# Optimization experiments

Measured on AMD Instinct MI355X. Metric: run time of the kernel, lower is better.

Reference implementation:

```python
import jax, jax.numpy as jnp
import numpy as np

IN_MODES = (8, 8, 8, 8)
OUT_MODES = (8, 8, 8, 8)
R = 16
RANKS = (1, R, R, R, 1)
BATCH = 8192
PROD_IN = int(np.prod(IN_MODES))   # 4096
PROD_OUT = int(np.prod(OUT_MODES))  # 4096


def setup_inputs() -> dict:
    key = jax.random.key(0)
    ks = jax.random.split(key, 6)
    # matches reset_normal() init scale
    CONST = ((0.05 ** 2 / np.prod(RANKS)) ** (1.0 / (len(RANKS) - 1))) ** 0.5
    P0 = jax.random.normal(ks[0], (OUT_MODES[0] * IN_MODES[0], R, 1), jnp.float32) * CONST
    P1 = jax.random.normal(ks[1], (OUT_MODES[1] * IN_MODES[1], R, R), jnp.float32) * CONST
    P2 = jax.random.normal(ks[2], (OUT_MODES[2] * IN_MODES[2], R, R), jnp.float32) * CONST
    P3 = jax.random.normal(ks[3], (OUT_MODES[3] * IN_MODES[3], R, 1), jnp.float32) * CONST
    bias = jnp.zeros((PROD_OUT,), jnp.float32)
    x = jax.random.normal(ks[5], (BATCH, PROD_IN), jnp.float32)
    return {"x": x, "P0": P0, "P1": P1, "P2": P2, "P3": P3, "bias": bias}


def _cayley(P):
    # Batched Cayley transform: Q = (I - A) @ inv(I + A), A skew from triu(P,1).
    # P: (n, r, r)
    T = jnp.triu(P, 1)
    A = T - jnp.swapaxes(T, -1, -2)
    I = jnp.eye(P.shape[-1], dtype=P.dtype)
    return jnp.einsum('nij,njk->nik', I - A, jnp.linalg.inv(I + A))


def _core(Q, o, m, r_in, r_out, first):
    # Q: (o*m, r, c) stacked in (j, k) order -> U: (r, o, m, c) as in getU
    r, c = Q.shape[1], Q.shape[2]
    U = Q.reshape(o, m, r, c).transpose(2, 0, 1, 3)  # (r, o, m, c)
    if first:
        U = jnp.swapaxes(U, 0, 3)  # (c=1, o, m, r)
    return U.reshape(o * r_out, m * r_in)  # G_i: (o_i * ranks[i+1], m_i * ranks[i])


def _build_cores(P0, P1, P2, P3):
    G0 = _core(P0, OUT_MODES[0], IN_MODES[0], RANKS[0], RANKS[1], True)
    G1 = _core(_cayley(P1), OUT_MODES[1], IN_MODES[1], RANKS[1], RANKS[2], False)
    G2 = _core(_cayley(P2), OUT_MODES[2], IN_MODES[2], RANKS[2], RANKS[3], False)
    G3 = _core(P3, OUT_MODES[3], IN_MODES[3], RANKS[3], RANKS[4], False)
    return [G0, G1, G2, G3]


def _tt_dot(x, G, bias):
    res = x.reshape(-1, PROD_IN).T  # (prod_in, B)
    for ii in range(4):
        res = res.reshape(RANKS[ii] * IN_MODES[ii], -1)
        res = G[ii] @ res                       # (o_i * r_{i+1}, rest)
        res = res.reshape(OUT_MODES[ii], -1).T  # rotate processed mode to back
    res = res.reshape(-1, PROD_OUT)
    return res + bias


def reference(x, P0, P1, P2, P3, bias):
    G = _build_cores(P0, P1, P2, P3)
    return _tt_dot(x, G, bias)
```

## Files before the change

kernel.cpp:

```cpp
#include <hip/hip_runtime.h>
#include <hip/hip_bf16.h>

typedef __attribute__((ext_vector_type(8))) short sh8;
typedef __attribute__((ext_vector_type(16))) float fx16;
typedef __attribute__((ext_vector_type(4))) unsigned int u32x4;

__device__ __forceinline__ unsigned short f2bits(float a) {
  union { __hip_bfloat16 h; unsigned short u; } c;
  c.h = __float2bfloat16(a);
  return c.u;
}
__device__ __forceinline__ unsigned int pkcvt(float a, float b) {
  unsigned int r;
  asm("v_cvt_pk_bf16_f32 %0, %1, %2" : "=v"(r) : "v"(a), "v"(b));
  return r;
}
__device__ __forceinline__ fx16 fzero16() {
  fx16 z;
  #pragma unroll
  for (int i = 0; i < 16; ++i) z[i] = 0.0f;
  return z;
}

__global__ void k_cayley(const float* __restrict__ P1, const float* __restrict__ P2,
                         float* __restrict__ Qout) {
  int t = blockIdx.x * blockDim.x + threadIdx.x;
  int mat = t >> 4;
  int row = t & 15;
  if (mat >= 128) return;
  const float* P = (mat < 64) ? (P1 + mat * 256) : (P2 + (mat - 64) * 256);
  float M[16], Rr[16];
  #pragma unroll
  for (int j = 0; j < 16; ++j) {
    float a = 0.0f;
    if (j > row) a = P[row * 16 + j];
    if (j < row) a = -P[j * 16 + row];
    float d = (j == row) ? 1.0f : 0.0f;
    M[j]  = d + a;
    Rr[j] = d - a;
  }
  int gbase = (threadIdx.x & 63) & ~15;
  #pragma unroll
  for (int k = 0; k < 16; ++k) {
    float pkk = __shfl(M[k], gbase + k);
    float inv = 1.0f / pkk;
    float pM[16], pR[16];
    #pragma unroll
    for (int j = 0; j < 16; ++j) {
      pM[j] = __shfl(M[j], gbase + k) * inv;
      pR[j] = __shfl(Rr[j], gbase + k) * inv;
    }
    if (row == k) {
      #pragma unroll
      for (int j = 0; j < 16; ++j) { M[j] = pM[j]; Rr[j] = pR[j]; }
    } else {
      float f = M[k];
      #pragma unroll
      for (int j = 0; j < 16; ++j) { M[j] -= f * pM[j]; Rr[j] -= f * pR[j]; }
    }
  }
  float* qo = Qout + mat * 256 + row * 16;
  #pragma unroll
  for (int j = 0; j < 16; ++j) qo[j] = Rr[j];
}

__global__ void k_build(const float* __restrict__ P0, const float* __restrict__ P3,
                        const float* __restrict__ Qbuf,
                        unsigned short* __restrict__ W1, unsigned short* __restrict__ W2) {
  int t = blockIdx.x * blockDim.x + threadIdx.x;
  if (t >= 131072) return;
  const float* Q1 = Qbuf;
  const float* Q2 = Qbuf + 16384;
  int e  = t & 65535;
  int r  = e & 7;
  int l  = (e >> 3) & 63;
  int kx = (e >> 9) & 3;
  int mt = (e >> 11) & 1;
  int t2 = (e >> 12) & 15;
  float acc = 0.0f;
  if (t < 65536) {
    int m = mt * 32 + (l & 31);
    int q = kx * 16 + ((l >> 5) << 3) + r;
    int j0 = m >> 3, j1 = m & 7, i0 = q >> 3, i1 = q & 7;
    #pragma unroll
    for (int t1 = 0; t1 < 16; ++t1) {
      float c0 = P0[(j0 * 8 + (t1 >> 1)) * 16 + ((t1 & 1) * 8 + i0)];
      int a1 = j1 * 16 + t2, u1 = t1 * 8 + i1;
      float c1 = Q1[((a1 & 7) * 8 + (u1 >> 4)) * 256 + (a1 >> 3) * 16 + (u1 & 15)];
      acc += c0 * c1;
    }
    W1[e] = f2bits(acc);
  } else {
    int n = mt * 32 + (l & 31);
    int s = kx * 16 + (r & 3) + 8 * (r >> 2) + 4 * (l >> 5);
    int j2 = n >> 3, j3 = n & 7, i2 = s >> 3, i3 = s & 7;
    #pragma unroll
    for (int t3 = 0; t3 < 16; ++t3) {
      int a2 = j2 * 16 + t3, u2 = t2 * 8 + i2;
      float c2 = Q2[((a2 & 7) * 8 + (u2 >> 4)) * 256 + (a2 >> 3) * 16 + (u2 & 15)];
      float c3 = P3[((t3 & 7) * 8 + i3) * 16 + (j3 * 2 + (t3 >> 3))];
      acc += c2 * c3;
    }
    W2[e] = f2bits(acc);
  }
}

__global__ __launch_bounds__(256, 2) void k_main(
    const float* __restrict__ x,
    const unsigned short* __restrict__ W1,
    const unsigned short* __restrict__ W2,
    const float* __restrict__ bias,
    float* __restrict__ out) {
  __shared__ __align__(16) char smem[4 * 8192 + 2 * 16384];
  char* XsT = smem;
  char* WL  = smem + 32768;

  const int tid  = threadIdx.x;
  const int lane = tid & 63;
  const int w    = tid >> 6;
  const int h    = lane >> 5;
  const int l31  = lane & 31;
  const int ep   = (w >> 1) * 2;
  const int mh   = w & 1;
  const size_t bbase = (size_t)blockIdx.x * 4;

  const char* w1c = (const char*)W1;
  const char* w2c = (const char*)W2;

  {
    char* dst = WL;
    #pragma unroll
    for (int c = 0; c < 4; ++c) {
      const char* src = (c < 2) ? (w1c + c * 4096) : (w2c + (c - 2) * 4096);
      src += w * 1024 + lane * 16;
      __builtin_amdgcn_global_load_lds((const unsigned int*)src,
                                       (unsigned int*)(dst + c * 4096 + w * 1024),
                                       16, 0, 0);
    }
  }

  {
    const int s = lane;
    const float* xb = x + (bbase + w) * 4096;
    const unsigned sw = ((unsigned)(s & 7)) << 4;
    char* base = XsT + w * 8192 + s * 128;
    #pragma unroll
    for (int c = 0; c < 4; ++c) {
      unsigned int d[8];
      #pragma unroll
      for (int jj = 0; jj < 8; ++jj) {
        float a  = xb[(c * 16 + 2 * jj + 0) * 64 + s];
        float bq = xb[(c * 16 + 2 * jj + 1) * 64 + s];
        d[jj] = pkcvt(a, bq);
      }
      u32x4 v0 = {d[0], d[1], d[2], d[3]};
      u32x4 v1 = {d[4], d[5], d[6], d[7]};
      *(u32x4*)(base + (((unsigned)(c * 32)) ^ sw))      = v0;
      *(u32x4*)(base + (((unsigned)(c * 32 + 16)) ^ sw)) = v1;
    }
  }
  asm volatile("s_waitcnt vmcnt(0)" ::: "memory");
  __syncthreads();

  sh8 af[2][2][4];
  #pragma unroll
  for (int e = 0; e < 2; ++e) {
    const char* myX = XsT + (ep + e) * 8192;
    #pragma unroll
    for (int st = 0; st < 2; ++st)
      #pragma unroll
      for (int kq = 0; kq < 4; ++kq) {
        int srow = st * 32 + l31;
        unsigned boff = (unsigned)srow * 128 +
                        (((unsigned)(kq * 32 + h * 16)) ^ (((unsigned)(srow & 7)) << 4));
        af[e][st][kq] = *(const sh8*)(myX + boff);
      }
  }

  const fx16 zc = fzero16();
  fx16 accO[2][2];
  accO[0][0] = zc; accO[0][1] = zc;
  accO[1][0] = zc; accO[1][1] = zc;

  #pragma unroll 1
  for (int t2 = 0; t2 < 16; ++t2) {
    char* cur = WL + (t2 & 1) * 16384;

    if (t2 < 15) {
      char* dst = WL + ((t2 + 1) & 1) * 16384;
      const size_t toff = (size_t)(t2 + 1) * 8192;
      #pragma unroll
      for (int c = 0; c < 4; ++c) {
        const char* src = (c < 2) ? (w1c + toff + c * 4096)
                                  : (w2c + toff + (c - 2) * 4096);
        src += w * 1024 + lane * 16;
        __builtin_amdgcn_global_load_lds((const unsigned int*)src,
                                         (unsigned int*)(dst + c * 4096 + w * 1024),
                                         16, 0, 0);
      }
    }

    sh8 b1[4];
    #pragma unroll
    for (int kq = 0; kq < 4; ++kq)
      b1[kq] = *(const sh8*)(cur + (((mh * 4 + kq) * 64 + lane) << 4));

    fx16 accY[2], accZ[2];
    __builtin_amdgcn_s_setprio(1);
    accY[0] = __builtin_amdgcn_mfma_f32_32x32x16_bf16(af[0][0][0], b1[0], zc, 0, 0, 0);
    accY[1] = __builtin_amdgcn_mfma_f32_32x32x16_bf16(af[0][1][0], b1[0], zc, 0, 0, 0);
    accZ[0] = __builtin_amdgcn_mfma_f32_32x32x16_bf16(af[1][0][0], b1[0], zc, 0, 0, 0);
    accZ[1] = __builtin_amdgcn_mfma_f32_32x32x16_bf16(af[1][1][0], b1[0], zc, 0, 0, 0);
    #pragma unroll
    for (int kq = 1; kq < 4; ++kq) {
      accY[0] = __builtin_amdgcn_mfma_f32_32x32x16_bf16(af[0][0][kq], b1[kq], accY[0], 0, 0, 0);
      accY[1] = __builtin_amdgcn_mfma_f32_32x32x16_bf16(af[0][1][kq], b1[kq], accY[1], 0, 0, 0);
      accZ[0] = __builtin_amdgcn_mfma_f32_32x32x16_bf16(af[1][0][kq], b1[kq], accZ[0], 0, 0, 0);
      accZ[1] = __builtin_amdgcn_mfma_f32_32x32x16_bf16(af[1][1][kq], b1[kq], accZ[1], 0, 0, 0);
    }
    __builtin_amdgcn_s_setprio(0);

    sh8 b2[2][4];
    #pragma unroll
    for (int nt = 0; nt < 2; ++nt)
      #pragma unroll
      for (int ks = 0; ks < 4; ++ks)
        b2[nt][ks] = *(const sh8*)(cur + 8192 + (((nt * 4 + ks) * 64 + lane) << 4));

    sh8 ga0[4], ga1[4];
    #pragma unroll
    for (int st = 0; st < 2; ++st) {
      fx16 Y = accY[st];
      union { u32x4 u; sh8 s8; } c0, c1;
      c0.u = (u32x4){pkcvt(Y[0], Y[1]),  pkcvt(Y[2], Y[3]),
                     pkcvt(Y[4], Y[5]),  pkcvt(Y[6], Y[7])};
      c1.u = (u32x4){pkcvt(Y[8], Y[9]),  pkcvt(Y[10], Y[11]),
                     pkcvt(Y[12], Y[13]), pkcvt(Y[14], Y[15])};
      ga0[st * 2 + 0] = c0.s8;
      ga0[st * 2 + 1] = c1.s8;
    }
    #pragma unroll
    for (int st = 0; st < 2; ++st) {
      fx16 Y = accZ[st];
      union { u32x4 u; sh8 s8; } c0, c1;
      c0.u = (u32x4){pkcvt(Y[0], Y[1]),  pkcvt(Y[2], Y[3]),
                     pkcvt(Y[4], Y[5]),  pkcvt(Y[6], Y[7])};
      c1.u = (u32x4){pkcvt(Y[8], Y[9]),  pkcvt(Y[10], Y[11]),
                     pkcvt(Y[12], Y[13]), pkcvt(Y[14], Y[15])};
      ga1[st * 2 + 0] = c0.s8;
      ga1[st * 2 + 1] = c1.s8;
    }

    __builtin_amdgcn_s_setprio(1);
    #pragma unroll
    for (int ks = 0; ks < 4; ++ks) {
      accO[0][0] = __builtin_amdgcn_mfma_f32_32x32x16_bf16(ga0[ks], b2[0][ks], accO[0][0], 0, 0, 0);
      accO[0][1] = __builtin_amdgcn_mfma_f32_32x32x16_bf16(ga0[ks], b2[1][ks], accO[0][1], 0, 0, 0);
      accO[1][0] = __builtin_amdgcn_mfma_f32_32x32x16_bf16(ga1[ks], b2[0][ks], accO[1][0], 0, 0, 0);
      accO[1][1] = __builtin_amdgcn_mfma_f32_32x32x16_bf16(ga1[ks], b2[1][ks], accO[1][1], 0, 0, 0);
    }
    __builtin_amdgcn_s_setprio(0);

    asm volatile("s_waitcnt vmcnt(0)" ::: "memory");
    __syncthreads();
  }

  #pragma unroll
  for (int e = 0; e < 2; ++e) {
    float* ob = out + (bbase + ep + e) * 4096;
    #pragma unroll
    for (int nt = 0; nt < 2; ++nt) {
      #pragma unroll
      for (int reg = 0; reg < 16; ++reg) {
        int m = mh * 32 + (reg & 3) + 8 * (reg >> 2) + 4 * h;
        int n = nt * 32 + l31;
        int o = m * 64 + n;
        ob[o] = accO[e][nt][reg] + bias[o];
      }
    }
  }
}

extern "C" void kernel_launch(void* const* d_in, const int* in_sizes, int n_in,
                              void* d_out, int out_size, void* d_ws, size_t ws_size,
                              hipStream_t stream) {
  (void)n_in; (void)out_size; (void)ws_size;
  const float* x    = (const float*)d_in[0];
  const float* P0   = (const float*)d_in[1];
  const float* P1   = (const float*)d_in[2];
  const float* P2   = (const float*)d_in[3];
  const float* P3   = (const float*)d_in[4];
  const float* bias = (const float*)d_in[5];
  float* out = (float*)d_out;

  float* Qbuf = (float*)d_ws;
  unsigned short* W1 = (unsigned short*)((char*)d_ws + 131072);
  unsigned short* W2 = (unsigned short*)((char*)d_ws + 262144);

  k_cayley<<<8, 256, 0, stream>>>(P1, P2, Qbuf);
  k_build<<<512, 256, 0, stream>>>(P0, P3, Qbuf, W1, W2);

  int batch = in_sizes[0] / 4096;
  k_main<<<batch / 4, 256, 0, stream>>>(x, W1, W2, bias, out);
}
```

Before: 137.7 us.

## Software-pipeline second-stage MFMAs across iterations and reload X fragments from LDS

The main loop is restructured so the second-stage GEMM (accO updates) for tile t-1 is interleaved with the first-stage GEMM for tile t, with a peeled prologue and epilogue. This gives independent MFMA chains to overlap instead of back-to-back dependent ones. The A fragments of X are no longer held in registers for the whole kernel; they are re-read from LDS each iteration per batch element, which lowers register pressure but adds LDS traffic. The b2 fragments are carried across iterations in registers.

```diff
diff --git a/kernel.cpp b/kernel.cpp
--- a/kernel.cpp
+++ b/kernel.cpp
@@ -162,37 +162,34 @@
   asm volatile("s_waitcnt vmcnt(0)" ::: "memory");
   __syncthreads();
 
-  sh8 af[2][2][4];
-  #pragma unroll
-  for (int e = 0; e < 2; ++e) {
-    const char* myX = XsT + (ep + e) * 8192;
-    #pragma unroll
-    for (int st = 0; st < 2; ++st)
-      #pragma unroll
-      for (int kq = 0; kq < 4; ++kq) {
-        int srow = st * 32 + l31;
-        unsigned boff = (unsigned)srow * 128 +
-                        (((unsigned)(kq * 32 + h * 16)) ^ (((unsigned)(srow & 7)) << 4));
-        af[e][st][kq] = *(const sh8*)(myX + boff);
-      }
-  }
+  unsigned aoff[2][4];
+  #pragma unroll
+  for (int st = 0; st < 2; ++st)
+    #pragma unroll
+    for (int kq = 0; kq < 4; ++kq) {
+      int srow = st * 32 + l31;
+      aoff[st][kq] = (unsigned)srow * 128 +
+                     (((unsigned)(kq * 32 + h * 16)) ^ (((unsigned)(srow & 7)) << 4));
+    }
+  const char* myX0 = XsT + (ep + 0) * 8192;
+  const char* myX1 = XsT + (ep + 1) * 8192;
 
   const fx16 zc = fzero16();
   fx16 accO[2][2];
   accO[0][0] = zc; accO[0][1] = zc;
   accO[1][0] = zc; accO[1][1] = zc;
 
-  #pragma unroll 1
-  for (int t2 = 0; t2 < 16; ++t2) {
-    char* cur = WL + (t2 & 1) * 16384;
-
-    if (t2 < 15) {
-      char* dst = WL + ((t2 + 1) & 1) * 16384;
-      const size_t toff = (size_t)(t2 + 1) * 8192;
+  sh8 ga0[4], ga1[4];
+  sh8 b2h[2][4];
+
+  {
+    char* cur = WL;
+    {
+      char* dst = WL + 16384;
       #pragma unroll
       for (int c = 0; c < 4; ++c) {
-        const char* src = (c < 2) ? (w1c + toff + c * 4096)
-                                  : (w2c + toff + (c - 2) * 4096);
+        const char* src = (c < 2) ? (w1c + 8192 + c * 4096)
+                                  : (w2c + 8192 + (c - 2) * 4096);
         src += w * 1024 + lane * 16;
         __builtin_amdgcn_global_load_lds((const unsigned int*)src,
                                          (unsigned int*)(dst + c * 4096 + w * 1024),
@@ -205,29 +202,46 @@
     for (int kq = 0; kq < 4; ++kq)
       b1[kq] = *(const sh8*)(cur + (((mh * 4 + kq) * 64 + lane) << 4));
 
+    sh8 afc[2][4];
+    #pragma unroll
+    for (int st = 0; st < 2; ++st)
+      #pragma unroll
+      for (int kq = 0; kq < 4; ++kq)
+        afc[st][kq] = *(const sh8*)(myX0 + aoff[st][kq]);
+
     fx16 accY[2], accZ[2];
     __builtin_amdgcn_s_setprio(1);
-    accY[0] = __builtin_amdgcn_mfma_f32_32x32x16_bf16(af[0][0][0], b1[0], zc, 0, 0, 0);
-    accY[1] = __builtin_amdgcn_mfma_f32_32x32x16_bf16(af[0][1][0], b1[0], zc, 0, 0, 0);
-    accZ[0] = __builtin_amdgcn_mfma_f32_32x32x16_bf16(af[1][0][0], b1[0], zc, 0, 0, 0);
-    accZ[1] = __builtin_amdgcn_mfma_f32_32x32x16_bf16(af[1][1][0], b1[0], zc, 0, 0, 0);
+    accY[0] = __builtin_amdgcn_mfma_f32_32x32x16_bf16(afc[0][0], b1[0], zc, 0, 0, 0);
+    accY[1] = __builtin_amdgcn_mfma_f32_32x32x16_bf16(afc[1][0], b1[0], zc, 0, 0, 0);
     #pragma unroll
     for (int kq = 1; kq < 4; ++kq) {
-      accY[0] = __builtin_amdgcn_mfma_f32_32x32x16_bf16(af[0][0][kq], b1[kq], accY[0], 0, 0, 0);
-      accY[1] = __builtin_amdgcn_mfma_f32_32x32x16_bf16(af[0][1][kq], b1[kq], accY[1], 0, 0, 0);
-      accZ[0] = __builtin_amdgcn_mfma_f32_32x32x16_bf16(af[1][0][kq], b1[kq], accZ[0], 0, 0, 0);
-      accZ[1] = __builtin_amdgcn_mfma_f32_32x32x16_bf16(af[1][1][kq], b1[kq], accZ[1], 0, 0, 0);
+      accY[0] = __builtin_amdgcn_mfma_f32_32x32x16_bf16(afc[0][kq], b1[kq], accY[0], 0, 0, 0);
+      accY[1] = __builtin_amdgcn_mfma_f32_32x32x16_bf16(afc[1][kq], b1[kq], accY[1], 0, 0, 0);
     }
     __builtin_amdgcn_s_setprio(0);
 
-    sh8 b2[2][4];
+    #pragma unroll
+    for (int st = 0; st < 2; ++st)
+      #pragma unroll
+      for (int kq = 0; kq < 4; ++kq)
+        afc[st][kq] = *(const sh8*)(myX1 + aoff[st][kq]);
+
+    __builtin_amdgcn_s_setprio(1);
+    accZ[0] = __builtin_amdgcn_mfma_f32_32x32x16_bf16(afc[0][0], b1[0], zc, 0, 0, 0);
+    accZ[1] = __builtin_amdgcn_mfma_f32_32x32x16_bf16(afc[1][0], b1[0], zc, 0, 0, 0);
+    #pragma unroll
+    for (int kq = 1; kq < 4; ++kq) {
+      accZ[0] = __builtin_amdgcn_mfma_f32_32x32x16_bf16(afc[0][kq], b1[kq], accZ[0], 0, 0, 0);
+      accZ[1] = __builtin_amdgcn_mfma_f32_32x32x16_bf16(afc[1][kq], b1[kq], accZ[1], 0, 0, 0);
+    }
+    __builtin_amdgcn_s_setprio(0);
+
     #pragma unroll
     for (int nt = 0; nt < 2; ++nt)
       #pragma unroll
       for (int ks = 0; ks < 4; ++ks)
-        b2[nt][ks] = *(const sh8*)(cur + 8192 + (((nt * 4 + ks) * 64 + lane) << 4));
-
-    sh8 ga0[4], ga1[4];
+        b2h[nt][ks] = *(const sh8*)(cur + 8192 + (((nt * 4 + ks) * 64 + lane) << 4));
+
     #pragma unroll
     for (int st = 0; st < 2; ++st) {
       fx16 Y = accY[st];
@@ -251,19 +265,117 @@
       ga1[st * 2 + 1] = c1.s8;
     }
 
-    __builtin_amdgcn_s_setprio(1);
-    #pragma unroll
-    for (int ks = 0; ks < 4; ++ks) {
-      accO[0][0] = __builtin_amdgcn_mfma_f32_32x32x16_bf16(ga0[ks], b2[0][ks], accO[0][0], 0, 0, 0);
-      accO[0][1] = __builtin_amdgcn_mfma_f32_32x32x16_bf16(ga0[ks], b2[1][ks], accO[0][1], 0, 0, 0);
-      accO[1][0] = __builtin_amdgcn_mfma_f32_32x32x16_bf16(ga1[ks], b2[0][ks], accO[1][0], 0, 0, 0);
-      accO[1][1] = __builtin_amdgcn_mfma_f32_32x32x16_bf16(ga1[ks], b2[1][ks], accO[1][1], 0, 0, 0);
-    }
-    __builtin_amdgcn_s_setprio(0);
-
     asm volatile("s_waitcnt vmcnt(0)" ::: "memory");
     __syncthreads();
   }
+
+  #pragma unroll 1
+  for (int t2 = 1; t2 < 16; ++t2) {
+    char* cur = WL + (t2 & 1) * 16384;
+
+    if (t2 < 15) {
+      char* dst = WL + ((t2 + 1) & 1) * 16384;
+      const size_t toff = (size_t)(t2 + 1) * 8192;
+      #pragma unroll
+      for (int c = 0; c < 4; ++c) {
+        const char* src = (c < 2) ? (w1c + toff + c * 4096)
+                                  : (w2c + toff + (c - 2) * 4096);
+        src += w * 1024 + lane * 16;
+        __builtin_amdgcn_global_load_lds((const unsigned int*)src,
+                                         (unsigned int*)(dst + c * 4096 + w * 1024),
+                                         16, 0, 0);
+      }
+    }
+
+    sh8 b1[4];
+    #pragma unroll
+    for (int kq = 0; kq < 4; ++kq)
+      b1[kq] = *(const sh8*)(cur + (((mh * 4 + kq) * 64 + lane) << 4));
+
+    sh8 afc[2][4];
+    #pragma unroll
+    for (int st = 0; st < 2; ++st)
+      #pragma unroll
+      for (int kq = 0; kq < 4; ++kq)
+        afc[st][kq] = *(const sh8*)(myX0 + aoff[st][kq]);
+
+    fx16 accY[2], accZ[2];
+    __builtin_amdgcn_s_setprio(1);
+    accO[0][0] = __builtin_amdgcn_mfma_f32_32x32x16_bf16(ga0[0], b2h[0][0], accO[0][0], 0, 0, 0);
+    accO[0][1] = __builtin_amdgcn_mfma_f32_32x32x16_bf16(ga0[0], b2h[1][0], accO[0][1], 0, 0, 0);
+    accY[0]    = __builtin_amdgcn_mfma_f32_32x32x16_bf16(afc[0][0], b1[0], zc, 0, 0, 0);
+    accY[1]    = __builtin_amdgcn_mfma_f32_32x32x16_bf16(afc[1][0], b1[0], zc, 0, 0, 0);
+    #pragma unroll
+    for (int k = 1; k < 4; ++k) {
+      accO[0][0] = __builtin_amdgcn_mfma_f32_32x32x16_bf16(ga0[k], b2h[0][k], accO[0][0], 0, 0, 0);
+      accO[0][1] = __builtin_amdgcn_mfma_f32_32x32x16_bf16(ga0[k], b2h[1][k], accO[0][1], 0, 0, 0);
+      accY[0]    = __builtin_amdgcn_mfma_f32_32x32x16_bf16(afc[0][k], b1[k], accY[0], 0, 0, 0);
+      accY[1]    = __builtin_amdgcn_mfma_f32_32x32x16_bf16(afc[1][k], b1[k], accY[1], 0, 0, 0);
+    }
+    __builtin_amdgcn_s_setprio(0);
+
+    #pragma unroll
+    for (int st = 0; st < 2; ++st)
+      #pragma unroll
+      for (int kq = 0; kq < 4; ++kq)
+        afc[st][kq] = *(const sh8*)(myX1 + aoff[st][kq]);
+
+    __builtin_amdgcn_s_setprio(1);
+    accO[1][0] = __builtin_amdgcn_mfma_f32_32x32x16_bf16(ga1[0], b2h[0][0], accO[1][0], 0, 0, 0);
+    accO[1][1] = __builtin_amdgcn_mfma_f32_32x32x16_bf16(ga1[0], b2h[1][0], accO[1][1], 0, 0, 0);
+    accZ[0]    = __builtin_amdgcn_mfma_f32_32x32x16_bf16(afc[0][0], b1[0], zc, 0, 0, 0);
+    accZ[1]    = __builtin_amdgcn_mfma_f32_32x32x16_bf16(afc[1][0], b1[0], zc, 0, 0, 0);
+    #pragma unroll
+    for (int k = 1; k < 4; ++k) {
+      accO[1][0] = __builtin_amdgcn_mfma_f32_32x32x16_bf16(ga1[k], b2h[0][k], accO[1][0], 0, 0, 0);
+      accO[1][1] = __builtin_amdgcn_mfma_f32_32x32x16_bf16(ga1[k], b2h[1][k], accO[1][1], 0, 0, 0);
+      accZ[0]    = __builtin_amdgcn_mfma_f32_32x32x16_bf16(afc[0][k], b1[k], accZ[0], 0, 0, 0);
+      accZ[1]    = __builtin_amdgcn_mfma_f32_32x32x16_bf16(afc[1][k], b1[k], accZ[1], 0, 0, 0);
+    }
+    __builtin_amdgcn_s_setprio(0);
+
+    #pragma unroll
+    for (int nt = 0; nt < 2; ++nt)
+      #pragma unroll
+      for (int ks = 0; ks < 4; ++ks)
+        b2h[nt][ks] = *(const sh8*)(cur + 8192 + (((nt * 4 + ks) * 64 + lane) << 4));
+
+    #pragma unroll
+    for (int st = 0; st < 2; ++st) {
+      fx16 Y = accY[st];
+      union { u32x4 u; sh8 s8; } c0, c1;
+      c0.u = (u32x4){pkcvt(Y[0], Y[1]),  pkcvt(Y[2], Y[3]),
+                     pkcvt(Y[4], Y[5]),  pkcvt(Y[6], Y[7])};
+      c1.u = (u32x4){pkcvt(Y[8], Y[9]),  pkcvt(Y[10], Y[11]),
+                     pkcvt(Y[12], Y[13]), pkcvt(Y[14], Y[15])};
+      ga0[st * 2 + 0] = c0.s8;
+      ga0[st * 2 + 1] = c1.s8;
+    }
+    #pragma unroll
+    for (int st = 0; st < 2; ++st) {
+      fx16 Y = accZ[st];
+      union { u32x4 u; sh8 s8; } c0, c1;
+      c0.u = (u32x4){pkcvt(Y[0], Y[1]),  pkcvt(Y[2], Y[3]),
+                     pkcvt(Y[4], Y[5]),  pkcvt(Y[6], Y[7])};
+      c1.u = (u32x4){pkcvt(Y[8], Y[9]),  pkcvt(Y[10], Y[11]),
+                     pkcvt(Y[12], Y[13]), pkcvt(Y[14], Y[15])};
+      ga1[st * 2 + 0] = c0.s8;
+      ga1[st * 2 + 1] = c1.s8;
+    }
+
+    asm volatile("s_waitcnt vmcnt(0)" ::: "memory");
+    __syncthreads();
+  }
+
+  __builtin_amdgcn_s_setprio(1);
+  #pragma unroll
+  for (int ks = 0; ks < 4; ++ks) {
+    accO[0][0] = __builtin_amdgcn_mfma_f32_32x32x16_bf16(ga0[ks], b2h[0][ks], accO[0][0], 0, 0, 0);
+    accO[0][1] = __builtin_amdgcn_mfma_f32_32x32x16_bf16(ga0[ks], b2h[1][ks], accO[0][1], 0, 0, 0);
+    accO[1][0] = __builtin_amdgcn_mfma_f32_32x32x16_bf16(ga1[ks], b2h[0][ks], accO[1][0], 0, 0, 0);
+    accO[1][1] = __builtin_amdgcn_mfma_f32_32x32x16_bf16(ga1[ks], b2h[1][ks], accO[1][1], 0, 0, 0);
+  }
+  __builtin_amdgcn_s_setprio(0);
 
   #pragma unroll
   for (int e = 0; e < 2; ++e) {
```

After: 150.5 us. 9.3% more time.
